# Performance work log

Measured on AMD Instinct MI355X. Metric: run time of the kernel, lower is better.

## Reference

```python
import jax, jax.numpy as jnp
import numpy as np


def _resize_axis(x, axis, out_size):
    # PyTorch bilinear interpolate, align_corners=False, no antialias (half-pixel centers)
    in_size = x.shape[axis]
    src = (jnp.arange(out_size) + 0.5) * (in_size / out_size) - 0.5
    src = jnp.clip(src, 0.0, in_size - 1.0)
    lo = jnp.floor(src).astype(jnp.int32)
    hi = jnp.minimum(lo + 1, in_size - 1)
    w = (src - lo).astype(x.dtype)
    shp = [1] * x.ndim
    shp[axis] = out_size
    w = w.reshape(shp)
    return jnp.take(x, lo, axis=axis) * (1 - w) + jnp.take(x, hi, axis=axis) * w


def _bilinear(x, h, w):
    return _resize_axis(_resize_axis(x, 2, h), 3, w)


def _unfold3(x):
    # F.unfold(kernel_size=3, padding=1) -> [B, C, 9, H*W], kernel offsets row-major
    B, C, H, W = x.shape
    xp = jnp.pad(x, ((0, 0), (0, 0), (1, 1), (1, 1)))
    pats = jnp.stack([xp[:, :, dy:dy + H, dx:dx + W] for dy in range(3) for dx in range(3)], axis=2)
    return pats.reshape(B, C, 9, H * W)


def setup_inputs() -> dict:
    key = jax.random.key(0)
    ks = jax.random.split(key, 7)
    B, C, H, W = 4, 64, 192, 192
    return {
        "x": jax.random.normal(ks[0], (B, C, H, W), jnp.float32),
        "gn_weight": jnp.ones((C,), jnp.float32) + 0.1 * jax.random.normal(ks[1], (C,), jnp.float32),
        "gn_bias": 0.1 * jax.random.normal(ks[2], (C,), jnp.float32),
        "w1": jax.random.normal(ks[3], (2 * C, C), jnp.float32) / np.sqrt(C).astype(np.float32),
        "b1": 0.01 * jax.random.normal(ks[4], (2 * C,), jnp.float32),
        "w2": jax.random.normal(ks[5], (C, 2 * C), jnp.float32) / np.sqrt(2 * C).astype(np.float32),
        "b2": 0.01 * jax.random.normal(ks[6], (C,), jnp.float32),
    }


def reference(x, gn_weight, gn_bias, w1, b1, w2, b2):
    B, C, H, W = x.shape
    MIN_CONN, MAX_CONN, THRESHOLD, POWER = 1, 16, 0.3, 2
    KSQ = 9
    K_MAX = min(MAX_CONN, KSQ)
    EPS_NORM = 1e-12

    x_down = _bilinear(x, H // 2, W // 2)
    x_du = _bilinear(x_down, H, W)
    df = jnp.abs(x - x_du).sum(1, keepdims=True)            # [B,1,H,W]
    dmin = df.reshape(B, -1).min(1).reshape(B, 1, 1, 1)
    dmax = df.reshape(B, -1).max(1).reshape(B, 1, 1, 1)
    dfp = ((df - dmin) / (dmax - dmin + 1e-8)) ** POWER
    mask = (dfp > THRESHOLD).astype(x.dtype)
    conn = MIN_CONN + jnp.clip(jnp.round(dfp * (MAX_CONN - MIN_CONN)), 0) * mask
    counts = conn.reshape(B, H * W)                          # [B,HW]
    process = counts > 1

    # ---- per-pixel cosine similarity to 3x3 neighborhood ----
    patches = _unfold3(x)                                    # [B,C,9,HW]
    x_flat = x.reshape(B, C, H * W)
    xn = x_flat / jnp.maximum(jnp.linalg.norm(x_flat, axis=1, keepdims=True), EPS_NORM)
    pn = patches / jnp.maximum(jnp.linalg.norm(patches, axis=1, keepdims=True), EPS_NORM)
    sim = jnp.einsum('bcn,bckn->bkn', xn, pn)                # [B,9,HW]

    # ---- adaptive top-k (k = min(count, 9)) + exp-softmax weighted sum of raw patches ----
    order = jnp.argsort(-sim, axis=1)                        # descending over the 9 neighbors
    sim_s = jnp.take_along_axis(sim, order, axis=1)
    pat_s = jnp.take_along_axis(patches, jnp.broadcast_to(order[:, None], patches.shape), axis=2)
    k = jnp.minimum(counts, K_MAX)                           # [B,HW]
    keep = (jnp.arange(KSQ)[None, :, None] < k[:, None, :]).astype(x.dtype)
    wts = jnp.exp(sim_s) * keep
    wts = wts / jnp.maximum(wts.sum(1, keepdims=True), EPS_NORM)
    weighted = jnp.einsum('bckn,bkn->bcn', pat_s, wts)       # [B,C,HW]
    output = jnp.where(process[:, None, :], weighted, x_flat).reshape(B, C, H, W)

    # ---- GroupNorm(32, C) on identity ----
    G = 32
    xg = x.reshape(B, G, C // G, H, W)
    mu = xg.mean((2, 3, 4), keepdims=True)
    var = xg.var((2, 3, 4), keepdims=True)
    nx = ((xg - mu) / jnp.sqrt(var + 1e-5)).reshape(B, C, H, W)
    norm_x = nx * gn_weight[None, :, None, None] + gn_bias[None, :, None, None]

    enhanced = output + norm_x
    # ---- conv_ffn: 1x1 conv C->2C, ReLU, 1x1 conv 2C->C ----
    h1 = jax.nn.relu(jnp.einsum('oc,bchw->bohw', w1, enhanced) + b1[None, :, None, None])
    ffn = jnp.einsum('oc,bchw->bohw', w2, h1) + b2[None, :, None, None]
    return enhanced + ffn
```

## Files before the change

kernel.cpp:

```cpp
#include <hip/hip_runtime.h>
#include <hip/hip_bf16.h>

#define BB 4
#define CC 64
#define HH 192
#define WW 192
#define HWSZ (HH*WW)
#define HD 96
#define WD 96
#define GG 32
#define FTH 512
#define FPX 128
#define FBPB (HWSZ/FPX)
#define PBLK 128
#define BPB (HWSZ/PBLK)

typedef short short8 __attribute__((ext_vector_type(8)));
typedef float f32x4  __attribute__((ext_vector_type(4)));

__device__ __forceinline__ unsigned short f2bf(float f) {
    unsigned u = __float_as_uint(f);
    return (unsigned short)((u + 0x7FFFu + ((u >> 16) & 1u)) >> 16);
}
__device__ __forceinline__ float bf2f(unsigned short s) {
    return __uint_as_float(((unsigned)s) << 16);
}
__device__ __forceinline__ unsigned pk2(float a, float b) {
    return (unsigned)f2bf(a) | ((unsigned)f2bf(b) << 16);
}
__device__ __forceinline__ short8 u4s8(uint4 u) {
    union { uint4 a; short8 b; } cvt; cvt.a = u; return cvt.b;
}

__device__ __forceinline__ int swz1152(int bid) {
    return (bid & 7) * 144 + (bid >> 3);
}

__global__ __launch_bounds__(512) void k_init(const float* __restrict__ w1,
                                              const float* __restrict__ w2,
                                              unsigned* __restrict__ wf,
                                              float* __restrict__ gnacc,
                                              unsigned* __restrict__ mm) {
    int tid = threadIdx.x;
    if (blockIdx.x == 0) {
        if (tid < 256) gnacc[tid] = 0.f;
        if (tid < 2*BB) mm[tid] = (tid & 1) ? 0u : 0x7F800000u;
    }
    int i = blockIdx.x*512 + tid;
    if (i < 4096) {
        float2 v = ((const float2*)w1)[i];
        int j = i >> 5, cp = i & 31, c0 = cp << 1;
        int fi = ((j >> 4) << 1) + (c0 >> 5);
        int ln = (((c0 & 31) >> 3) << 4) + (j & 15);
        wf[fi*256 + ln*4 + (cp & 3)] = pk2(v.x, v.y);
    } else {
        int i2 = i - 4096;
        float2 v = ((const float2*)w2)[i2];
        int c = i2 >> 6, jp = i2 & 63, j0 = jp << 1;
        int fi = ((j0 >> 5) << 2) + (c >> 4);
        int ln = (((j0 & 31) >> 3) << 4) + (c & 15);
        wf[4096 + fi*256 + ln*4 + (jp & 3)] = pk2(v.x, v.y);
    }
}

__global__ __launch_bounds__(256) void k_pre(const float* __restrict__ x,
                                             float* __restrict__ df,
                                             float* __restrict__ nrm,
                                             float* __restrict__ gnacc,
                                             unsigned* __restrict__ mm) {
    __shared__ float sgn[64];
    __shared__ float wmn[4], wmx[4];
    int tid = threadIdx.x;
    if (tid < 64) sgn[tid] = 0.f;
    __syncthreads();

    int virt = swz1152(blockIdx.x);
    int b = virt / BPB;
    int pb = (virt % BPB) * PBLK;
    int wave = tid >> 6, lane = tid & 63;
    int oct = lane >> 3, grp = lane & 7;
    int p0 = pb + wave*32 + grp*4;
    int h = p0 / WW, w0 = p0 % WW;

    float hs = fminf(fmaxf(0.5f*(float)h - 0.25f, 0.f), 95.f);
    int hl = (int)hs; int hh2 = min(hl+1, 95); float fh = hs - (float)hl;
    int r0 = 2*hl, r1 = 2*hh2;

    int t0 = min(max(w0/2 - 1, 0), 92);
    float wc[4][4];
    #pragma unroll
    for (int i = 0; i < 4; ++i) {
        float wsr = fminf(fmaxf(0.5f*(float)(w0+i) - 0.25f, 0.f), 95.f);
        int wl = (int)wsr; int wh = min(wl+1, 95); float fw = wsr - (float)wl;
        int kl = wl - t0, kh = wh - t0;
        #pragma unroll
        for (int k = 0; k < 4; ++k)
            wc[i][k] = ((k==kl) ? (1.f-fw) : 0.f) + ((k==kh) ? fw : 0.f);
    }

    const float* xb = x + (size_t)b*CC*HWSZ;
    float d[4]  = {0.f,0.f,0.f,0.f};
    float qn[4] = {0.f,0.f,0.f,0.f};
    float gs[4] = {0.f,0.f,0.f,0.f};
    float gq[4] = {0.f,0.f,0.f,0.f};
    #pragma unroll
    for (int cc = 0; cc < 8; ++cc) {
        const float* pc = xb + (size_t)(oct*8 + cc)*HWSZ;
        float4 xc = *(const float4*)(pc + h*WW + w0);
        const float* pa = pc + r0*WW + 2*t0;
        const float* pq = pc + r1*WW + 2*t0;
        float T[4];
        #pragma unroll
        for (int k = 0; k < 4; ++k) {
            float2 a0 = *(const float2*)(pa + 2*k);
            float2 a1 = *(const float2*)(pa + WW + 2*k);
            float2 c0 = *(const float2*)(pq + 2*k);
            float2 c1 = *(const float2*)(pq + WW + 2*k);
            float xdA = 0.25f*((a0.x + a1.x) + (a0.y + a1.y));
            float xdB = 0.25f*((c0.x + c1.x) + (c0.y + c1.y));
            T[k] = (1.f-fh)*xdA + fh*xdB;
        }
        float xv[4] = {xc.x, xc.y, xc.z, xc.w};
        float sch = 0.f, qch = 0.f;
        #pragma unroll
        for (int i = 0; i < 4; ++i) {
            float du = (wc[i][0]*T[0] + wc[i][1]*T[1]) + (wc[i][2]*T[2] + wc[i][3]*T[3]);
            d[i] += fabsf(xv[i] - du);
            float x2 = xv[i]*xv[i];
            qn[i] += x2;
            sch += xv[i];
            qch += x2;
        }
        gs[cc>>1] += sch;
        gq[cc>>1] += qch;
    }
    #pragma unroll
    for (int o = 8; o <= 32; o <<= 1) {
        #pragma unroll
        for (int i = 0; i < 4; ++i) {
            d[i]  += __shfl_xor(d[i], o);
            qn[i] += __shfl_xor(qn[i], o);
        }
    }
    if (oct == 0) {
        *(float4*)(df  + (size_t)b*HWSZ + p0) = make_float4(d[0], d[1], d[2], d[3]);
        *(float4*)(nrm + (size_t)b*HWSZ + p0) =
            make_float4(sqrtf(qn[0]), sqrtf(qn[1]), sqrtf(qn[2]), sqrtf(qn[3]));
    }
    float mn = fminf(fminf(d[0], d[1]), fminf(d[2], d[3]));
    float mx = fmaxf(fmaxf(d[0], d[1]), fmaxf(d[2], d[3]));
    #pragma unroll
    for (int o = 1; o < 64; o <<= 1) {
        mn = fminf(mn, __shfl_xor(mn, o));
        mx = fmaxf(mx, __shfl_xor(mx, o));
    }
    if (lane == 0) { wmn[wave] = mn; wmx[wave] = mx; }
    #pragma unroll
    for (int o = 1; o <= 4; o <<= 1) {
        #pragma unroll
        for (int j = 0; j < 4; ++j) {
            gs[j] += __shfl_xor(gs[j], o);
            gq[j] += __shfl_xor(gq[j], o);
        }
    }
    if (grp == 0) {
        #pragma unroll
        for (int j = 0; j < 4; ++j) {
            atomicAdd(&sgn[2*(oct*4+j)],   gs[j]);
            atomicAdd(&sgn[2*(oct*4+j)+1], gq[j]);
        }
    }
    __syncthreads();
    if (tid < 64) atomicAdd(&gnacc[(size_t)b*64 + tid], sgn[tid]);
    if (tid == 0) {
        float bmn = fminf(fminf(wmn[0], wmn[1]), fminf(wmn[2], wmn[3]));
        float bmx = fmaxf(fmaxf(wmx[0], wmx[1]), fmaxf(wmx[2], wmx[3]));
        atomicMin(&mm[2*b],   __float_as_uint(bmn));
        atomicMax(&mm[2*b+1], __float_as_uint(bmx));
    }
}

__global__ __launch_bounds__(FTH, 4) void k_fused(const float* __restrict__ x,
                                                  const float* __restrict__ df,
                                                  const float* __restrict__ nrm,
                                                  const unsigned* __restrict__ mm,
                                                  const float* __restrict__ gnacc,
                                                  const float* __restrict__ gw,
                                                  const float* __restrict__ gb,
                                                  const unsigned* __restrict__ wf,
                                                  const float* __restrict__ b1,
                                                  const float* __restrict__ b2,
                                                  float* __restrict__ out) {
    __shared__ __align__(16) unsigned char lds[24576];
    unsigned* se = (unsigned*)lds;
    unsigned* sh = (unsigned*)(lds + 16384);
    float* gnv = (float*)(lds + 16384);

    int tid = threadIdx.x;
    int wv = tid >> 6, lane = tid & 63;
    int q = lane >> 4, m = lane & 15;

    int virt = swz1152(blockIdx.x);
    int b = virt / FBPB;
    int pb = (virt % FBPB) * FPX;
    int pxl = wv*16 + m;
    int p = pb + pxl;
    int h = p / WW, w = p % WW;
    int cbase = q*16;

    if (tid < 32) {
        float n = 2.f*HWSZ;
        float mu  = gnacc[(size_t)b*64 + 2*tid] / n;
        float var = gnacc[(size_t)b*64 + 2*tid + 1] / n - mu*mu;
        gnv[2*tid]   = mu;
        gnv[2*tid+1] = rsqrtf(var + 1e-5f);
    }
    __syncthreads();

    float dmin = __uint_as_float(mm[2*b]);
    float dmax = __uint_as_float(mm[2*b+1]);
    float dfp = (df[b*HWSZ+p] - dmin) / (dmax - dmin + 1e-8f);
    dfp = dfp * dfp;
    bool maskv = dfp > 0.3f;
    float conn = 1.f + (maskv ? fmaxf(rintf(dfp * 15.f), 0.f) : 0.f);
    bool process = conn > 1.f;
    int kk = (int)fminf(conn, 9.f);

    const float* xb = x + (size_t)b*CC*HWSZ + p;
    const int dhv[9] = {-1,-1,-1, 0,0,0, 1,1,1};
    const int dwv[9] = {-1, 0, 1,-1,0,1,-1,0,1};
    bool valid[9]; int offc[9];
    #pragma unroll
    for (int j = 0; j < 9; ++j) {
        int hn = h + dhv[j], wn = w + dwv[j];
        valid[j] = (hn >= 0) && (hn < HH) && (wn >= 0) && (wn < WW);
        offc[j] = valid[j] ? (dhv[j]*WW + dwv[j]) : 0;
    }
    float wtc[9];
    #pragma unroll
    for (int j = 0; j < 9; ++j) wtc[j] = 0.f;

    if (process) {
        float dot[9];
        #pragma unroll
        for (int j = 0; j < 9; ++j) dot[j] = 0.f;
        #pragma unroll 2
        for (int cc = 0; cc < 16; ++cc) {
            const float* pc = xb + (size_t)(cbase + cc)*HWSZ;
            float xc = pc[0];
            #pragma unroll
            for (int j = 0; j < 9; ++j)
                dot[j] += xc * pc[offc[j]];
        }
        #pragma unroll
        for (int j = 0; j < 9; ++j) {
            dot[j] += __shfl_xor(dot[j], 16);
            dot[j] += __shfl_xor(dot[j], 32);
        }
        float nc = fmaxf(nrm[b*HWSZ+p], 1e-12f);
        float sim[9];
        #pragma unroll
        for (int j = 0; j < 9; ++j) {
            float nj = fmaxf(nrm[b*HWSZ+p+offc[j]], 1e-12f);
            sim[j] = valid[j] ? dot[j] / (nc * nj) : 0.f;
        }
        float S = 0.f;
        float wt[9];
        #pragma unroll
        for (int j = 0; j < 9; ++j) {
            int rank = 0;
            #pragma unroll
            for (int l = 0; l < 9; ++l)
                rank += (sim[l] > sim[j]) || (sim[l] == sim[j] && l < j);
            float ex = (rank < kk) ? expf(sim[j]) : 0.f;
            wt[j] = ex; S += ex;
        }
        float inv = 1.f / fmaxf(S, 1e-12f);
        #pragma unroll
        for (int j = 0; j < 9; ++j)
            wtc[j] = valid[j] ? wt[j] * inv : 0.f;
    }

    float e[16];
    for (int cc = 0; cc < 16; ++cc) {
        int c = cbase + cc;
        const float* pc = xb + (size_t)c*HWSZ;
        float xc = pc[0];
        float oc;
        if (process) {
            float a = 0.f;
            #pragma unroll
            for (int j = 0; j < 9; ++j)
                a += wtc[j] * pc[offc[j]];
            oc = a;
        } else oc = xc;
        int g = c >> 1;
        float mu = gnv[2*g], is = gnv[2*g+1];
        e[cc] = oc + (xc - mu) * is * gw[c] + gb[c];
    }

    {
        int kc = q >> 1, qo = q & 1;
        unsigned* dst = se + (wv*2 + kc)*256;
        int la = 32*qo + m;
        uint4 ua, ub;
        ua.x = pk2(e[0],e[1]);  ua.y = pk2(e[2],e[3]);
        ua.z = pk2(e[4],e[5]);  ua.w = pk2(e[6],e[7]);
        ub.x = pk2(e[8],e[9]);  ub.y = pk2(e[10],e[11]);
        ub.z = pk2(e[12],e[13]); ub.w = pk2(e[14],e[15]);
        *(uint4*)(dst + la*4)      = ua;
        *(uint4*)(dst + (la+16)*4) = ub;
    }
    __syncthreads();

    const unsigned* wf1g = wf;
    const unsigned* wf2g = wf + 4096;
    int n16 = m;
    float b1v[8], b2v[4];
    #pragma unroll
    for (int nt = 0; nt < 8; ++nt) b1v[nt] = b1[nt*16 + n16];
    #pragma unroll
    for (int n2 = 0; n2 < 4; ++n2) b2v[n2] = b2[n2*16 + n16];

    uint4 a0 = *(uint4*)(se + (wv*2+0)*256 + lane*4);
    uint4 a1 = *(uint4*)(se + (wv*2+1)*256 + lane*4);
    f32x4 D1[8];
    #pragma unroll
    for (int nt = 0; nt < 8; ++nt) D1[nt] = (f32x4){0.f,0.f,0.f,0.f};
    #pragma unroll
    for (int nt = 0; nt < 8; ++nt) {
        uint4 bk0 = *(const uint4*)(wf1g + (nt*2+0)*256 + lane*4);
        uint4 bk1 = *(const uint4*)(wf1g + (nt*2+1)*256 + lane*4);
        D1[nt] = __builtin_amdgcn_mfma_f32_16x16x32_bf16(u4s8(a0), u4s8(bk0), D1[nt], 0, 0, 0);
        D1[nt] = __builtin_amdgcn_mfma_f32_16x16x32_bf16(u4s8(a1), u4s8(bk1), D1[nt], 0, 0, 0);
    }
    f32x4 D2[4];
    #pragma unroll
    for (int n2 = 0; n2 < 4; ++n2) D2[n2] = (f32x4){0.f,0.f,0.f,0.f};
    unsigned* shwv = sh + wv*256;
    unsigned short* shw = (unsigned short*)shwv;
    for (int kc2 = 0; kc2 < 4; ++kc2) {
        #pragma unroll
        for (int h2 = 0; h2 < 2; ++h2) {
            int nt = kc2*2 + h2;
            #pragma unroll
            for (int r = 0; r < 4; ++r) {
                float hval = fmaxf(D1[nt][r] + b1v[nt], 0.f);
                int mrow = q*4 + r;
                int k = h2*16 + n16;
                shw[((k >> 3)*16 + mrow)*8 + (k & 7)] = f2bf(hval);
            }
        }
        uint4 ah = *(uint4*)(shwv + lane*4);
        #pragma unroll
        for (int n2 = 0; n2 < 4; ++n2) {
            uint4 bb = *(const uint4*)(wf2g + (kc2*4 + n2)*256 + lane*4);
            D2[n2] = __builtin_amdgcn_mfma_f32_16x16x32_bf16(u4s8(ah), u4s8(bb), D2[n2], 0, 0, 0);
        }
    }
    float vals[4][4];
    unsigned short* seu = (unsigned short*)se;
    #pragma unroll
    for (int n2 = 0; n2 < 4; ++n2) {
        int c = n2*16 + n16;
        int kc = c >> 5, qq = (c & 31) >> 3, jj = c & 7;
        #pragma unroll
        for (int r = 0; r < 4; ++r) {
            int pxt = q*4 + r;
            float resid = bf2f(seu[((wv*2+kc)*64 + qq*16 + pxt)*8 + jj]);
            vals[n2][r] = D2[n2][r] + resid + b2v[n2];
        }
    }
    __syncthreads();

    float* stg = (float*)lds;
    float* outb = out + (size_t)b*CC*HWSZ;
    #pragma unroll
    for (int g = 0; g < 2; ++g) {
        #pragma unroll
        for (int hn2 = 0; hn2 < 2; ++hn2) {
            int n2 = 2*g + hn2;
            int row = (n2 & 1)*16 + n16;
            float4 v4 = make_float4(vals[n2][0], vals[n2][1], vals[n2][2], vals[n2][3]);
            *(float4*)&stg[row*132 + wv*16 + q*4] = v4;
        }
        __syncthreads();
        #pragma unroll
        for (int rr = 0; rr < 2; ++rr) {
            int r0 = (wv*2 + rr)*2 + (lane >> 5);
            int px4 = (lane & 31) * 4;
            float4 v = *(float4*)&stg[r0*132 + px4];
            *(float4*)&outb[(size_t)(g*32 + r0)*HWSZ + pb + px4] = v;
        }
        if (g == 0) __syncthreads();
    }
}

extern "C" void kernel_launch(void* const* d_in, const int* in_sizes, int n_in,
                              void* d_out, int out_size, void* d_ws, size_t ws_size,
                              hipStream_t stream) {
    const float* x  = (const float*)d_in[0];
    const float* gw = (const float*)d_in[1];
    const float* gb = (const float*)d_in[2];
    const float* w1 = (const float*)d_in[3];
    const float* b1 = (const float*)d_in[4];
    const float* w2 = (const float*)d_in[5];
    const float* b2 = (const float*)d_in[6];
    float* out = (float*)d_out;

    float* df    = (float*)d_ws;
    float* nrm   = df + 147456;
    float* gnacc = nrm + 147456;
    unsigned* mm = (unsigned*)(gnacc + 256);
    unsigned* wf = mm + 8;

    k_init <<<16, 512, 0, stream>>>(w1, w2, wf, gnacc, mm);
    k_pre  <<<BB*BPB, 256, 0, stream>>>(x, df, nrm, gnacc, mm);
    k_fused<<<BB*FBPB, FTH, 0, stream>>>(x, df, nrm, mm, gnacc, gw, gb,
                                         wf, b1, b2, out);
}
```

Measured before the change: 188.7 us.

## Restructure pre-pass per image row and precompute neighbor dot products

```diff
diff --git a/kernel.cpp b/kernel.cpp
--- a/kernel.cpp
+++ b/kernel.cpp
@@ -12,8 +12,6 @@
 #define FTH 512
 #define FPX 128
 #define FBPB (HWSZ/FPX)
-#define PBLK 128
-#define BPB (HWSZ/PBLK)
 
 typedef short short8 __attribute__((ext_vector_type(8)));
 typedef float f32x4  __attribute__((ext_vector_type(4)));
@@ -63,126 +61,144 @@
     }
 }
 
-__global__ __launch_bounds__(256) void k_pre(const float* __restrict__ x,
-                                             float* __restrict__ df,
-                                             float* __restrict__ nrm,
-                                             float* __restrict__ gnacc,
-                                             unsigned* __restrict__ mm) {
+__global__ __launch_bounds__(256, 3) void k_pre(const float* __restrict__ x,
+                                                float* __restrict__ df,
+                                                float* __restrict__ nrm,
+                                                float* __restrict__ dots,
+                                                float* __restrict__ gnacc,
+                                                unsigned* __restrict__ mm) {
+    __shared__ __align__(16) float rb[2][4][WW];
+    __shared__ float Tt[96];
     __shared__ float sgn[64];
-    __shared__ float wmn[4], wmx[4];
+    __shared__ float wred[8];
+
     int tid = threadIdx.x;
+    int lane = tid & 63, wv = tid >> 6;
     if (tid < 64) sgn[tid] = 0.f;
-    __syncthreads();
-
-    int virt = swz1152(blockIdx.x);
-    int b = virt / BPB;
-    int pb = (virt % BPB) * PBLK;
-    int wave = tid >> 6, lane = tid & 63;
-    int oct = lane >> 3, grp = lane & 7;
-    int p0 = pb + wave*32 + grp*4;
-    int h = p0 / WW, w0 = p0 % WW;
+
+    int virt = (blockIdx.x & 7) * 96 + (blockIdx.x >> 3);
+    int b = virt / HH, h = virt % HH;
 
     float hs = fminf(fmaxf(0.5f*(float)h - 0.25f, 0.f), 95.f);
     int hl = (int)hs; int hh2 = min(hl+1, 95); float fh = hs - (float)hl;
-    int r0 = 2*hl, r1 = 2*hh2;
-
-    int t0 = min(max(w0/2 - 1, 0), 92);
-    float wc[4][4];
-    #pragma unroll
-    for (int i = 0; i < 4; ++i) {
-        float wsr = fminf(fmaxf(0.5f*(float)(w0+i) - 0.25f, 0.f), 95.f);
-        int wl = (int)wsr; int wh = min(wl+1, 95); float fw = wsr - (float)wl;
-        int kl = wl - t0, kh = wh - t0;
-        #pragma unroll
-        for (int k = 0; k < 4; ++k)
-            wc[i][k] = ((k==kl) ? (1.f-fw) : 0.f) + ((k==kh) ? fw : 0.f);
-    }
-
+    int R[4] = {2*hl, 2*hl+1, 2*hh2, 2*hh2+1};
+    int su = 0, cs = 0, sd = 0;
+    #pragma unroll
+    for (int s = 3; s >= 0; --s) {
+        if (R[s] == h-1) su = s;
+        if (R[s] == h)   cs = s;
+        if (R[s] == h+1) sd = s;
+    }
     const float* xb = x + (size_t)b*CC*HWSZ;
-    float d[4]  = {0.f,0.f,0.f,0.f};
-    float qn[4] = {0.f,0.f,0.f,0.f};
-    float gs[4] = {0.f,0.f,0.f,0.f};
-    float gq[4] = {0.f,0.f,0.f,0.f};
-    #pragma unroll
-    for (int cc = 0; cc < 8; ++cc) {
-        const float* pc = xb + (size_t)(oct*8 + cc)*HWSZ;
-        float4 xc = *(const float4*)(pc + h*WW + w0);
-        const float* pa = pc + r0*WW + 2*t0;
-        const float* pq = pc + r1*WW + 2*t0;
-        float T[4];
-        #pragma unroll
-        for (int k = 0; k < 4; ++k) {
-            float2 a0 = *(const float2*)(pa + 2*k);
-            float2 a1 = *(const float2*)(pa + WW + 2*k);
-            float2 c0 = *(const float2*)(pq + 2*k);
-            float2 c1 = *(const float2*)(pq + WW + 2*k);
-            float xdA = 0.25f*((a0.x + a1.x) + (a0.y + a1.y));
-            float xdB = 0.25f*((c0.x + c1.x) + (c0.y + c1.y));
-            T[k] = (1.f-fh)*xdA + fh*xdB;
-        }
-        float xv[4] = {xc.x, xc.y, xc.z, xc.w};
-        float sch = 0.f, qch = 0.f;
-        #pragma unroll
-        for (int i = 0; i < 4; ++i) {
-            float du = (wc[i][0]*T[0] + wc[i][1]*T[1]) + (wc[i][2]*T[2] + wc[i][3]*T[3]);
-            d[i] += fabsf(xv[i] - du);
-            float x2 = xv[i]*xv[i];
-            qn[i] += x2;
-            sch += xv[i];
-            qch += x2;
-        }
-        gs[cc>>1] += sch;
-        gq[cc>>1] += qch;
-    }
-    #pragma unroll
-    for (int o = 8; o <= 32; o <<= 1) {
-        #pragma unroll
-        for (int i = 0; i < 4; ++i) {
-            d[i]  += __shfl_xor(d[i], o);
-            qn[i] += __shfl_xor(qn[i], o);
-        }
-    }
-    if (oct == 0) {
-        *(float4*)(df  + (size_t)b*HWSZ + p0) = make_float4(d[0], d[1], d[2], d[3]);
-        *(float4*)(nrm + (size_t)b*HWSZ + p0) =
-            make_float4(sqrtf(qn[0]), sqrtf(qn[1]), sqrtf(qn[2]), sqrtf(qn[3]));
-    }
-    float mn = fminf(fminf(d[0], d[1]), fminf(d[2], d[3]));
-    float mx = fmaxf(fmaxf(d[0], d[1]), fmaxf(d[2], d[3]));
-    #pragma unroll
-    for (int o = 1; o < 64; o <<= 1) {
+
+    bool stager = tid < 192;
+    int slot = (tid / 48) & 3, col4 = (tid % 48) * 4;
+    const float* srow = xb + (size_t)R[slot]*WW + col4;
+
+    bool isT  = tid < 96;
+    bool ispx = (tid >= 96) && (tid < 192);
+    int j  = tid - 96;
+    int w0 = 2*j, w1 = 2*j + 1;
+    int cl = max(w0 - 1, 0), cr = min(w1 + 1, WW - 1);
+
+    float dA[9], dB[9];
+    #pragma unroll
+    for (int k = 0; k < 9; ++k) { dA[k] = 0.f; dB[k] = 0.f; }
+    float dfA = 0.f, dfB = 0.f, sAcc = 0.f, qAcc = 0.f;
+
+    float4 v;
+    if (stager) {
+        v = *(const float4*)(srow);
+        *(float4*)&rb[0][slot][col4] = v;
+        v = *(const float4*)(srow + HWSZ);
+    }
+    __syncthreads();
+
+    for (int c = 0; c < CC; ++c) {
+        int cur = c & 1;
+        if (isT) {
+            float2 r0 = *(const float2*)&rb[cur][0][2*tid];
+            float2 r1 = *(const float2*)&rb[cur][1][2*tid];
+            float2 r2 = *(const float2*)&rb[cur][2][2*tid];
+            float2 r3 = *(const float2*)&rb[cur][3][2*tid];
+            float xdl = 0.25f*((r0.x + r1.x) + (r0.y + r1.y));
+            float xdh = 0.25f*((r2.x + r3.x) + (r2.y + r3.y));
+            Tt[tid] = (1.f - fh)*xdl + fh*xdh;
+        }
+        if (stager && c+1 < CC) *(float4*)&rb[cur^1][slot][col4] = v;
+        __syncthreads();
+        if (stager && c+2 < CC) v = *(const float4*)(srow + (size_t)(c+2)*HWSZ);
+
+        if (ispx) {
+            float2 c01 = *(const float2*)&rb[cur][cs][w0];
+            float xc0 = c01.x, xc1 = c01.y;
+            float du0 = (j == 0)  ? Tt[0]  : 0.25f*Tt[j-1] + 0.75f*Tt[j];
+            float du1 = (j == 95) ? Tt[95] : 0.75f*Tt[j]   + 0.25f*Tt[j+1];
+            dfA += fabsf(xc0 - du0);
+            dfB += fabsf(xc1 - du1);
+            int rows[3] = {su, cs, sd};
+            #pragma unroll
+            for (int r = 0; r < 3; ++r) {
+                int s = rows[r];
+                float vl = rb[cur][s][cl];
+                float2 v01 = *(const float2*)&rb[cur][s][w0];
+                float vr = rb[cur][s][cr];
+                dA[3*r+0] += xc0*vl;     dA[3*r+1] += xc0*v01.x;  dA[3*r+2] += xc0*v01.y;
+                dB[3*r+0] += xc1*v01.x;  dB[3*r+1] += xc1*v01.y;  dB[3*r+2] += xc1*vr;
+            }
+            sAcc += xc0 + xc1;
+            qAcc += xc0*xc0 + xc1*xc1;
+        }
+        if (c & 1) {
+            float s_ = sAcc, q_ = qAcc;
+            #pragma unroll
+            for (int o = 1; o <= 32; o <<= 1) {
+                s_ += __shfl_xor(s_, o);
+                q_ += __shfl_xor(q_, o);
+            }
+            if (lane == 0) {
+                atomicAdd(&sgn[c-1], s_);
+                atomicAdd(&sgn[c],   q_);
+            }
+            sAcc = 0.f; qAcc = 0.f;
+        }
+        __syncthreads();
+    }
+
+    if (ispx) {
+        size_t base = (size_t)b*HWSZ + h*WW + w0;
+        *(float2*)&df[base]  = make_float2(dfA, dfB);
+        *(float2*)&nrm[base] = make_float2(sqrtf(dA[4]), sqrtf(dB[4]));
+        if (dots) {
+            #pragma unroll
+            for (int jj = 0; jj < 9; ++jj)
+                *(float2*)&dots[(size_t)(b*9 + jj)*HWSZ + h*WW + w0] =
+                    make_float2(dA[jj], dB[jj]);
+        }
+    }
+    float mn = ispx ? fminf(dfA, dfB) : 3.4e38f;
+    float mx = ispx ? fmaxf(dfA, dfB) : 0.f;
+    #pragma unroll
+    for (int o = 1; o <= 32; o <<= 1) {
         mn = fminf(mn, __shfl_xor(mn, o));
         mx = fmaxf(mx, __shfl_xor(mx, o));
     }
-    if (lane == 0) { wmn[wave] = mn; wmx[wave] = mx; }
-    #pragma unroll
-    for (int o = 1; o <= 4; o <<= 1) {
-        #pragma unroll
-        for (int j = 0; j < 4; ++j) {
-            gs[j] += __shfl_xor(gs[j], o);
-            gq[j] += __shfl_xor(gq[j], o);
-        }
-    }
-    if (grp == 0) {
-        #pragma unroll
-        for (int j = 0; j < 4; ++j) {
-            atomicAdd(&sgn[2*(oct*4+j)],   gs[j]);
-            atomicAdd(&sgn[2*(oct*4+j)+1], gq[j]);
-        }
-    }
+    if (lane == 0) { wred[wv] = mn; wred[4+wv] = mx; }
     __syncthreads();
     if (tid < 64) atomicAdd(&gnacc[(size_t)b*64 + tid], sgn[tid]);
     if (tid == 0) {
-        float bmn = fminf(fminf(wmn[0], wmn[1]), fminf(wmn[2], wmn[3]));
-        float bmx = fmaxf(fmaxf(wmx[0], wmx[1]), fmaxf(wmx[2], wmx[3]));
+        float bmn = fminf(fminf(wred[0], wred[1]), fminf(wred[2], wred[3]));
+        float bmx = fmaxf(fmaxf(wred[4], wred[5]), fmaxf(wred[6], wred[7]));
         atomicMin(&mm[2*b],   __float_as_uint(bmn));
         atomicMax(&mm[2*b+1], __float_as_uint(bmx));
     }
 }
 
+template<int USE_DOTS>
 __global__ __launch_bounds__(FTH, 4) void k_fused(const float* __restrict__ x,
                                                   const float* __restrict__ df,
                                                   const float* __restrict__ nrm,
+                                                  const float* __restrict__ dots,
                                                   const unsigned* __restrict__ mm,
                                                   const float* __restrict__ gnacc,
                                                   const float* __restrict__ gw,
@@ -231,54 +247,61 @@
     const int dwv[9] = {-1, 0, 1,-1,0,1,-1,0,1};
     bool valid[9]; int offc[9];
     #pragma unroll
-    for (int j = 0; j < 9; ++j) {
-        int hn = h + dhv[j], wn = w + dwv[j];
-        valid[j] = (hn >= 0) && (hn < HH) && (wn >= 0) && (wn < WW);
-        offc[j] = valid[j] ? (dhv[j]*WW + dwv[j]) : 0;
+    for (int jj = 0; jj < 9; ++jj) {
+        int hn = h + dhv[jj], wn = w + dwv[jj];
+        valid[jj] = (hn >= 0) && (hn < HH) && (wn >= 0) && (wn < WW);
+        offc[jj] = valid[jj] ? (dhv[jj]*WW + dwv[jj]) : 0;
     }
     float wtc[9];
     #pragma unroll
-    for (int j = 0; j < 9; ++j) wtc[j] = 0.f;
+    for (int jj = 0; jj < 9; ++jj) wtc[jj] = 0.f;
 
     if (process) {
         float dot[9];
-        #pragma unroll
-        for (int j = 0; j < 9; ++j) dot[j] = 0.f;
-        #pragma unroll 2
-        for (int cc = 0; cc < 16; ++cc) {
-            const float* pc = xb + (size_t)(cbase + cc)*HWSZ;
-            float xc = pc[0];
-            #pragma unroll
-            for (int j = 0; j < 9; ++j)
-                dot[j] += xc * pc[offc[j]];
-        }
-        #pragma unroll
-        for (int j = 0; j < 9; ++j) {
-            dot[j] += __shfl_xor(dot[j], 16);
-            dot[j] += __shfl_xor(dot[j], 32);
+        if (USE_DOTS) {
+            const float* dp = dots + (size_t)b*9*HWSZ + p;
+            #pragma unroll
+            for (int jj = 0; jj < 9; ++jj)
+                dot[jj] = dp[(size_t)jj*HWSZ];
+        } else {
+            #pragma unroll
+            for (int jj = 0; jj < 9; ++jj) dot[jj] = 0.f;
+            #pragma unroll 2
+            for (int cc = 0; cc < 16; ++cc) {
+                const float* pc = xb + (size_t)(cbase + cc)*HWSZ;
+                float xc = pc[0];
+                #pragma unroll
+                for (int jj = 0; jj < 9; ++jj)
+                    dot[jj] += xc * pc[offc[jj]];
+            }
+            #pragma unroll
+            for (int jj = 0; jj < 9; ++jj) {
+                dot[jj] += __shfl_xor(dot[jj], 16);
+                dot[jj] += __shfl_xor(dot[jj], 32);
+            }
         }
         float nc = fmaxf(nrm[b*HWSZ+p], 1e-12f);
         float sim[9];
         #pragma unroll
-        for (int j = 0; j < 9; ++j) {
-            float nj = fmaxf(nrm[b*HWSZ+p+offc[j]], 1e-12f);
-            sim[j] = valid[j] ? dot[j] / (nc * nj) : 0.f;
+        for (int jj = 0; jj < 9; ++jj) {
+            float nj = fmaxf(nrm[b*HWSZ+p+offc[jj]], 1e-12f);
+            sim[jj] = valid[jj] ? dot[jj] / (nc * nj) : 0.f;
         }
         float S = 0.f;
         float wt[9];
         #pragma unroll
-        for (int j = 0; j < 9; ++j) {
+        for (int jj = 0; jj < 9; ++jj) {
             int rank = 0;
             #pragma unroll
             for (int l = 0; l < 9; ++l)
-                rank += (sim[l] > sim[j]) || (sim[l] == sim[j] && l < j);
-            float ex = (rank < kk) ? expf(sim[j]) : 0.f;
-            wt[j] = ex; S += ex;
+                rank += (sim[l] > sim[jj]) || (sim[l] == sim[jj] && l < jj);
+            float ex = (rank < kk) ? expf(sim[jj]) : 0.f;
+            wt[jj] = ex; S += ex;
         }
         float inv = 1.f / fmaxf(S, 1e-12f);
         #pragma unroll
-        for (int j = 0; j < 9; ++j)
-            wtc[j] = valid[j] ? wt[j] * inv : 0.f;
+        for (int jj = 0; jj < 9; ++jj)
+            wtc[jj] = valid[jj] ? wt[jj] * inv : 0.f;
     }
 
     float e[16];
@@ -290,8 +313,8 @@
         if (process) {
             float a = 0.f;
             #pragma unroll
-            for (int j = 0; j < 9; ++j)
-                a += wtc[j] * pc[offc[j]];
+            for (int jj = 0; jj < 9; ++jj)
+                a += wtc[jj] * pc[offc[jj]];
             oc = a;
         } else oc = xc;
         int g = c >> 1;
@@ -389,8 +412,8 @@
         for (int rr = 0; rr < 2; ++rr) {
             int r0 = (wv*2 + rr)*2 + (lane >> 5);
             int px4 = (lane & 31) * 4;
-            float4 v = *(float4*)&stg[r0*132 + px4];
-            *(float4*)&outb[(size_t)(g*32 + r0)*HWSZ + pb + px4] = v;
+            float4 vv = *(float4*)&stg[r0*132 + px4];
+            *(float4*)&outb[(size_t)(g*32 + r0)*HWSZ + pb + px4] = vv;
         }
         if (g == 0) __syncthreads();
     }
@@ -413,9 +436,17 @@
     float* gnacc = nrm + 147456;
     unsigned* mm = (unsigned*)(gnacc + 256);
     unsigned* wf = mm + 8;
-
-    k_init <<<16, 512, 0, stream>>>(w1, w2, wf, gnacc, mm);
-    k_pre  <<<BB*BPB, 256, 0, stream>>>(x, df, nrm, gnacc, mm);
-    k_fused<<<BB*FBPB, FTH, 0, stream>>>(x, df, nrm, mm, gnacc, gw, gb,
-                                         wf, b1, b2, out);
-}
+    float* dots  = (float*)(wf + 8192);
+    const size_t NEED = (size_t)(147456*2 + 256 + 8 + 8192 + 9*147456) * 4;
+    bool big = ws_size >= NEED;
+    float* dotsArg = big ? dots : nullptr;
+
+    k_init<<<16, 512, 0, stream>>>(w1, w2, wf, gnacc, mm);
+    k_pre <<<BB*HH, 256, 0, stream>>>(x, df, nrm, dotsArg, gnacc, mm);
+    if (big)
+        k_fused<1><<<BB*FBPB, FTH, 0, stream>>>(x, df, nrm, dots, mm, gnacc,
+                                                gw, gb, wf, b1, b2, out);
+    else
+        k_fused<0><<<BB*FBPB, FTH, 0, stream>>>(x, df, nrm, nullptr, mm, gnacc,
+                                                gw, gb, wf, b1, b2, out);
+}
```

Result: slower. 209.9 us (+11.2%).
